# Kernel tuning notes

Hardware: AMD Instinct MI355X
Metric: run time of the kernel (lower is better)

Reference implementation:

```python
import jax, jax.numpy as jnp
import numpy as np

B, L, D = 2, 2048, 2048
NH, HD = 16, 128
SCALE = HD ** -0.5


def setup_inputs() -> dict:
    key = jax.random.key(0)
    ks = jax.random.split(key, 9)
    s = D ** -0.5  # roughly torch Linear init scale
    return {
        "hidden_states": jax.random.normal(ks[0], (B, L, D), dtype=jnp.float32),
        "Wq": jax.random.normal(ks[1], (NH * HD, D), dtype=jnp.float32) * s,
        "bq": jnp.zeros((NH * HD,), dtype=jnp.float32),
        "Wk": jax.random.normal(ks[2], (NH * HD, D), dtype=jnp.float32) * s,
        "bk": jnp.zeros((NH * HD,), dtype=jnp.float32),
        "Wv": jax.random.normal(ks[3], (NH * HD, D), dtype=jnp.float32) * s,
        "bv": jnp.zeros((NH * HD,), dtype=jnp.float32),
        "Wo": jax.random.normal(ks[4], (D, NH * HD), dtype=jnp.float32) * s,
        "bo": jnp.zeros((D,), dtype=jnp.float32),
    }


def reference(hidden_states, Wq, bq, Wk, bk, Wv, bv, Wo, bo):
    # projections (torch Linear: x @ W.T + b), split into heads: b s h d
    q = (hidden_states @ Wq.T + bq).reshape(B, L, NH, HD)
    k = (hidden_states @ Wk.T + bk).reshape(B, L, NH, HD)
    v = (hidden_states @ Wv.T + bv).reshape(B, L, NH, HD)
    # scores: [B, NH, L, L]
    scores = jnp.einsum("bqhd,bkhd->bhqk", q, k) * SCALE
    causal = jnp.tril(jnp.ones((L, L), dtype=bool))  # True = keep
    scores = jnp.where(causal, scores, jnp.float32(-jnp.inf))
    probs = jax.nn.softmax(scores, axis=-1)
    out = jnp.einsum("bhqk,bkhd->bqhd", probs, v).reshape(B, L, NH * HD)
    return out @ Wo.T + bo
```

## Files before the change

### kernel.cpp

```cpp
#include <hip/hip_runtime.h>

#define B_  2
#define L_  2048
#define D_  2048
#define NH_ 16
#define HD_ 128

typedef __bf16 bf16_t;
typedef __bf16 bf16x8 __attribute__((ext_vector_type(8)));
typedef __bf16 bf16x4 __attribute__((ext_vector_type(4)));
typedef float  f32x4  __attribute__((ext_vector_type(4)));

typedef const __attribute__((address_space(1))) void* gas_ptr;
typedef __attribute__((address_space(3))) void* las_ptr;

__device__ __forceinline__ void g2l16(const void* g, void* l) {
    __builtin_amdgcn_global_load_lds((gas_ptr)g, (las_ptr)l, 16, 0, 0);
}

__device__ __forceinline__ void raw_barrier() {
    asm volatile("s_barrier" ::: "memory");
}
__device__ __forceinline__ void wait_vm8() {
    asm volatile("s_waitcnt vmcnt(8)" ::: "memory");
}
__device__ __forceinline__ void wait_vm2() {
    asm volatile("s_waitcnt vmcnt(2)" ::: "memory");
}
__device__ __forceinline__ void wait_vm0() {
    asm volatile("s_waitcnt vmcnt(0)" ::: "memory");
}

__global__ __launch_bounds__(256) void cvt_all(const float* __restrict__ X,
                                               const float* __restrict__ Wq,
                                               const float* __restrict__ Wk,
                                               const float* __restrict__ Wv,
                                               const float* __restrict__ Wo,
                                               bf16_t* __restrict__ Xb,
                                               bf16_t* __restrict__ Wqkvb,
                                               bf16_t* __restrict__ Wob) {
    int i = blockIdx.x * 256 + threadIdx.x;
    const float* src;
    bf16_t* dst;
    int off;
    if (i < 2097152) { src = X; dst = Xb; off = i; }
    else {
        int j = i - 2097152;
        int w = j >> 20;
        off = j & 1048575;
        src = (w == 0) ? Wq : (w == 1) ? Wk : (w == 2) ? Wv : Wo;
        dst = (w == 3) ? Wob : Wqkvb + (size_t)w * 4194304;
    }
    float4 v = ((const float4*)src)[off];
    bf16x4 o;
    o[0] = (bf16_t)v.x; o[1] = (bf16_t)v.y; o[2] = (bf16_t)v.z; o[3] = (bf16_t)v.w;
    ((bf16x4*)dst)[off] = o;
}

__global__ __launch_bounds__(512, 2) void gemm_qk(const bf16_t* __restrict__ A,
                                                  const bf16_t* __restrict__ Bw,
                                                  const float* __restrict__ b0,
                                                  const float* __restrict__ b1,
                                                  bf16_t* __restrict__ QK) {
    constexpr int K  = D_;
    constexpr int BK = 64;
    constexpr int NT = K / BK;
    __shared__ __align__(16) bf16_t smem[65536];

    const int tid  = threadIdx.x;
    const int wave = tid >> 6, lane = tid & 63;
    const int quad = lane >> 4, l16 = lane & 15;
    const int tm = blockIdx.y * 256, tn = blockIdx.x * 256;
    const int seg = tn >> 11;

    const int srow = tid >> 3;
    const int sg   = (tid & 7) ^ (srow & 7);
    const bf16_t* Ag = A  + (size_t)(tm + srow) * K + sg * 8;
    const bf16_t* Bg = Bw + (size_t)(tn + srow) * K + sg * 8;
    const int ldsw = wave * 512;

    auto stageA = [&](int t, int h) {
        bf16_t* l = smem + (t & 1) * 32768 + h * 8192 + ldsw;
        const bf16_t* g = Ag + (size_t)h * 128 * K + t * BK;
        g2l16(g, l);
        g2l16(g + (size_t)64 * K, l + 4096);
    };
    auto stageB = [&](int t, int h) {
        bf16_t* l = smem + (t & 1) * 32768 + 16384 + h * 8192 + ldsw;
        const bf16_t* g = Bg + (size_t)h * 128 * K + t * BK;
        g2l16(g, l);
        g2l16(g + (size_t)64 * K, l + 4096);
    };

    f32x4 acc[8][4] = {};

    stageA(0, 0); stageA(0, 1); stageB(0, 0); stageB(0, 1);

    const int abase_w = (wave >> 2) * 8192;
    const int bbase_w = 16384 + ((wave >> 1) & 1) * 8192;
    const int brow0   = (wave & 1) * 64;

    for (int t = 0; t < NT; ++t) {
        const int p = t & 1;
        const bf16_t* Ah = smem + p * 32768 + abase_w;
        const bf16_t* Bh = smem + p * 32768 + bbase_w;
        bf16x8 af[4][2], bfr[2][2], bfr2[2][2];

        raw_barrier();
        if (t + 1 < NT) { stageA(t + 1, 0); wait_vm2(); }
        else wait_vm0();
        raw_barrier();

#pragma unroll
        for (int mb = 0; mb < 4; ++mb)
#pragma unroll
            for (int ks = 0; ks < 2; ++ks) {
                const int row = mb * 16 + l16;
                af[mb][ks] = *(const bf16x8*)(Ah + row * 64 + (((ks * 4 + quad) ^ (row & 7)) << 3));
            }
#pragma unroll
        for (int nb = 0; nb < 2; ++nb)
#pragma unroll
            for (int ks = 0; ks < 2; ++ks) {
                const int row = brow0 + nb * 16 + l16;
                bfr[nb][ks] = *(const bf16x8*)(Bh + row * 64 + (((ks * 4 + quad) ^ (row & 7)) << 3));
            }
        __builtin_amdgcn_s_setprio(1);
#pragma unroll
        for (int mb = 0; mb < 4; ++mb)
#pragma unroll
            for (int nb = 0; nb < 2; ++nb)
#pragma unroll
                for (int ks = 0; ks < 2; ++ks)
                    acc[mb][nb] = __builtin_amdgcn_mfma_f32_16x16x32_bf16(af[mb][ks], bfr[nb][ks], acc[mb][nb], 0, 0, 0);
        __builtin_amdgcn_s_setprio(0);

        if (t + 1 < NT) stageA(t + 1, 1);
#pragma unroll
        for (int nb = 0; nb < 2; ++nb)
#pragma unroll
            for (int ks = 0; ks < 2; ++ks) {
                const int row = brow0 + (nb + 2) * 16 + l16;
                bfr2[nb][ks] = *(const bf16x8*)(Bh + row * 64 + (((ks * 4 + quad) ^ (row & 7)) << 3));
            }
        raw_barrier();
        __builtin_amdgcn_s_setprio(1);
#pragma unroll
        for (int mb = 0; mb < 4; ++mb)
#pragma unroll
            for (int nb = 0; nb < 2; ++nb)
#pragma unroll
                for (int ks = 0; ks < 2; ++ks)
                    acc[mb][nb + 2] = __builtin_amdgcn_mfma_f32_16x16x32_bf16(af[mb][ks], bfr2[nb][ks], acc[mb][nb + 2], 0, 0, 0);
        __builtin_amdgcn_s_setprio(0);

        if (t + 1 < NT) stageB(t + 1, 0);
#pragma unroll
        for (int mb = 0; mb < 4; ++mb)
#pragma unroll
            for (int ks = 0; ks < 2; ++ks) {
                const int row = (mb + 4) * 16 + l16;
                af[mb][ks] = *(const bf16x8*)(Ah + row * 64 + (((ks * 4 + quad) ^ (row & 7)) << 3));
            }
        raw_barrier();
        __builtin_amdgcn_s_setprio(1);
#pragma unroll
        for (int mb = 0; mb < 4; ++mb)
#pragma unroll
            for (int nb = 0; nb < 2; ++nb)
#pragma unroll
                for (int ks = 0; ks < 2; ++ks)
                    acc[mb + 4][nb + 2] = __builtin_amdgcn_mfma_f32_16x16x32_bf16(af[mb][ks], bfr2[nb][ks], acc[mb + 4][nb + 2], 0, 0, 0);
        __builtin_amdgcn_s_setprio(0);

        if (t + 1 < NT) stageB(t + 1, 1);
#pragma unroll
        for (int nb = 0; nb < 2; ++nb)
#pragma unroll
            for (int ks = 0; ks < 2; ++ks) {
                const int row = brow0 + nb * 16 + l16;
                bfr[nb][ks] = *(const bf16x8*)(Bh + row * 64 + (((ks * 4 + quad) ^ (row & 7)) << 3));
            }
        raw_barrier();
        __builtin_amdgcn_s_setprio(1);
#pragma unroll
        for (int mb = 0; mb < 4; ++mb)
#pragma unroll
            for (int nb = 0; nb < 2; ++nb)
#pragma unroll
                for (int ks = 0; ks < 2; ++ks)
                    acc[mb + 4][nb] = __builtin_amdgcn_mfma_f32_16x16x32_bf16(af[mb][ks], bfr[nb][ks], acc[mb + 4][nb], 0, 0, 0);
        __builtin_amdgcn_s_setprio(0);
    }

    const int wm = (wave >> 2) * 128;
    const int wn = (wave & 3) * 64;
    const float* bias = (seg == 0) ? b0 : b1;
#pragma unroll
    for (int nb = 0; nb < 4; ++nb) {
        const int col = tn + wn + nb * 16 + l16;
        const float bv = bias[col & 2047];
#pragma unroll
        for (int mb = 0; mb < 8; ++mb) {
            const int row0 = tm + wm + mb * 16 + quad * 4;
#pragma unroll
            for (int r = 0; r < 4; ++r)
                QK[(size_t)(row0 + r) * 4096 + col] = (bf16_t)(acc[mb][nb][r] + bv);
        }
    }
}

__global__ __launch_bounds__(512, 2) void gemm_v(const bf16_t* __restrict__ A,
                                                 const bf16_t* __restrict__ Bv,
                                                 const float* __restrict__ b2,
                                                 bf16_t* __restrict__ Vt) {
    constexpr int K  = D_;
    constexpr int BK = 64;
    constexpr int NT = K / BK;
    __shared__ __align__(16) bf16_t smem[49152];

    const int tid  = threadIdx.x;
    const int wave = tid >> 6, lane = tid & 63;
    const int quad = lane >> 4, l16 = lane & 15;
    const int hx = blockIdx.x;
    const int tm = blockIdx.y * 256;
    const int wm = (wave >> 1) * 64;
    const int wn = (wave & 1) * 64;

    const int srow = tid >> 3;
    const int sg   = (tid & 7) ^ (srow & 7);
    const bf16_t* Ag = A  + (size_t)(tm + srow) * K + sg * 8;
    const bf16_t* Bg = Bv + (size_t)(hx * 128 + srow) * K + sg * 8;
    const int ldsw = wave * 512;

    auto stageVA = [&](int t, int q) {
        bf16_t* l = smem + (t & 1) * 24576 + q * 4096 + ldsw;
        g2l16(Ag + (size_t)q * 64 * K + t * BK, l);
    };
    auto stageVB = [&](int t, int q) {
        bf16_t* l = smem + (t & 1) * 24576 + 16384 + q * 4096 + ldsw;
        g2l16(Bg + (size_t)q * 64 * K + t * BK, l);
    };

    f32x4 acc[4][4] = {};

    stageVA(0, 0); stageVA(0, 1); stageVA(0, 2); stageVA(0, 3);
    stageVB(0, 0); stageVB(0, 1);

    for (int t = 0; t < NT; ++t) {
        const int p = t & 1;
        const bf16_t* Ah = smem + p * 24576;
        const bf16_t* Bl = smem + p * 24576 + 16384;
        bf16x8 af0[4], af1[4], bf0[2], bf1[2], bf2[2], bf3[2];

        raw_barrier();
        if (t + 1 < NT) { stageVA(t + 1, 0); stageVA(t + 1, 1); wait_vm2(); }
        else wait_vm0();
        raw_barrier();

#pragma unroll
        for (int mb = 0; mb < 4; ++mb) {
            const int row = wm + mb * 16 + l16;
            af0[mb] = *(const bf16x8*)(Ah + row * 64 + ((quad ^ (row & 7)) << 3));
        }
#pragma unroll
        for (int nb = 0; nb < 2; ++nb) {
            const int row = wn + nb * 16 + l16;
            bf0[nb] = *(const bf16x8*)(Bl + row * 64 + ((quad ^ (row & 7)) << 3));
        }
        __builtin_amdgcn_s_setprio(1);
#pragma unroll
        for (int mb = 0; mb < 4; ++mb)
#pragma unroll
            for (int nb = 0; nb < 2; ++nb)
                acc[mb][nb] = __builtin_amdgcn_mfma_f32_16x16x32_bf16(af0[mb], bf0[nb], acc[mb][nb], 0, 0, 0);
        __builtin_amdgcn_s_setprio(0);

        if (t + 1 < NT) { stageVA(t + 1, 2); stageVB(t + 1, 0); }
#pragma unroll
        for (int nb = 0; nb < 2; ++nb) {
            const int row = wn + (nb + 2) * 16 + l16;
            bf1[nb] = *(const bf16x8*)(Bl + row * 64 + ((quad ^ (row & 7)) << 3));
        }
        raw_barrier();
        __builtin_amdgcn_s_setprio(1);
#pragma unroll
        for (int mb = 0; mb < 4; ++mb)
#pragma unroll
            for (int nb = 0; nb < 2; ++nb)
                acc[mb][nb + 2] = __builtin_amdgcn_mfma_f32_16x16x32_bf16(af0[mb], bf1[nb], acc[mb][nb + 2], 0, 0, 0);
        __builtin_amdgcn_s_setprio(0);

        if (t + 1 < NT) { stageVA(t + 1, 3); stageVB(t + 1, 1); }
#pragma unroll
        for (int mb = 0; mb < 4; ++mb) {
            const int row = wm + mb * 16 + l16;
            af1[mb] = *(const bf16x8*)(Ah + row * 64 + (((4 + quad) ^ (row & 7)) << 3));
        }
#pragma unroll
        for (int nb = 0; nb < 2; ++nb) {
            const int row = wn + (nb + 2) * 16 + l16;
            bf2[nb] = *(const bf16x8*)(Bl + row * 64 + (((4 + quad) ^ (row & 7)) << 3));
        }
        raw_barrier();
        __builtin_amdgcn_s_setprio(1);
#pragma unroll
        for (int mb = 0; mb < 4; ++mb)
#pragma unroll
            for (int nb = 0; nb < 2; ++nb)
                acc[mb][nb + 2] = __builtin_amdgcn_mfma_f32_16x16x32_bf16(af1[mb], bf2[nb], acc[mb][nb + 2], 0, 0, 0);
        __builtin_amdgcn_s_setprio(0);

#pragma unroll
        for (int nb = 0; nb < 2; ++nb) {
            const int row = wn + nb * 16 + l16;
            bf3[nb] = *(const bf16x8*)(Bl + row * 64 + (((4 + quad) ^ (row & 7)) << 3));
        }
        raw_barrier();
        __builtin_amdgcn_s_setprio(1);
#pragma unroll
        for (int mb = 0; mb < 4; ++mb)
#pragma unroll
            for (int nb = 0; nb < 2; ++nb)
                acc[mb][nb] = __builtin_amdgcn_mfma_f32_16x16x32_bf16(af1[mb], bf3[nb], acc[mb][nb], 0, 0, 0);
        __builtin_amdgcn_s_setprio(0);
    }

    __syncthreads();
    bf16_t* Tw = smem + wave * 4096;
    const int b = tm >> 11;
    const int tokbase = tm & 2047;
#pragma unroll
    for (int nb = 0; nb < 4; ++nb) {
        const int dloc = nb * 16 + l16;
        const float bv = b2[hx * 128 + wn + dloc];
#pragma unroll
        for (int mb = 0; mb < 4; ++mb)
#pragma unroll
            for (int r = 0; r < 4; ++r) {
                const int tokl = mb * 16 + quad * 4 + r;
                Tw[dloc * 64 + ((((tokl >> 3) ^ (dloc & 7)) << 3) | (tokl & 7))] =
                    (bf16_t)(acc[mb][nb][r] + bv);
            }
    }
    const int dl = lane;
    bf16_t* gp = Vt + ((size_t)(b * NH_ + hx) * HD_ + wn + dl) * L_ + tokbase + wm;
#pragma unroll
    for (int c = 0; c < 8; ++c) {
        bf16x8 v = *(const bf16x8*)(Tw + dl * 64 + ((c ^ (dl & 7)) << 3));
        *(bf16x8*)(gp + c * 8) = v;
    }
}

__global__ __launch_bounds__(512, 2) void gemm_o(const bf16_t* __restrict__ A,
                                                 const bf16_t* __restrict__ Bw,
                                                 const float* __restrict__ bias,
                                                 float* __restrict__ C) {
    constexpr int K  = D_;
    constexpr int BK = 64;
    constexpr int NT = K / BK;
    __shared__ __align__(16) bf16_t smem[49152];

    const int tid  = threadIdx.x;
    const int wave = tid >> 6, lane = tid & 63;
    const int quad = lane >> 4, l16 = lane & 15;
    const int tn = blockIdx.x * 128;
    const int tm = blockIdx.y * 256;
    const int wm = (wave >> 1) * 64;
    const int wn = (wave & 1) * 64;

    const int srow = tid >> 3;
    const int sg   = (tid & 7) ^ (srow & 7);
    const bf16_t* Ag = A  + (size_t)(tm + srow) * K + sg * 8;
    const bf16_t* Bg = Bw + (size_t)(tn + srow) * K + sg * 8;
    const int ldsw = wave * 512;

    auto stageVA = [&](int t, int q) {
        bf16_t* l = smem + (t & 1) * 24576 + q * 4096 + ldsw;
        g2l16(Ag + (size_t)q * 64 * K + t * BK, l);
    };
    auto stageVB = [&](int t, int q) {
        bf16_t* l = smem + (t & 1) * 24576 + 16384 + q * 4096 + ldsw;
        g2l16(Bg + (size_t)q * 64 * K + t * BK, l);
    };

    f32x4 acc[4][4] = {};

    stageVA(0, 0); stageVA(0, 1); stageVA(0, 2); stageVA(0, 3);
    stageVB(0, 0); stageVB(0, 1);

    for (int t = 0; t < NT; ++t) {
        const int p = t & 1;
        const bf16_t* Ah = smem + p * 24576;
        const bf16_t* Bl = smem + p * 24576 + 16384;
        bf16x8 af0[4], af1[4], bf0[2], bf1[2], bf2[2], bf3[2];

        raw_barrier();
        if (t + 1 < NT) { stageVA(t + 1, 0); stageVA(t + 1, 1); wait_vm2(); }
        else wait_vm0();
        raw_barrier();

#pragma unroll
        for (int mb = 0; mb < 4; ++mb) {
            const int row = wm + mb * 16 + l16;
            af0[mb] = *(const bf16x8*)(Ah + row * 64 + ((quad ^ (row & 7)) << 3));
        }
#pragma unroll
        for (int nb = 0; nb < 2; ++nb) {
            const int row = wn + nb * 16 + l16;
            bf0[nb] = *(const bf16x8*)(Bl + row * 64 + ((quad ^ (row & 7)) << 3));
        }
        __builtin_amdgcn_s_setprio(1);
#pragma unroll
        for (int mb = 0; mb < 4; ++mb)
#pragma unroll
            for (int nb = 0; nb < 2; ++nb)
                acc[mb][nb] = __builtin_amdgcn_mfma_f32_16x16x32_bf16(af0[mb], bf0[nb], acc[mb][nb], 0, 0, 0);
        __builtin_amdgcn_s_setprio(0);

        if (t + 1 < NT) { stageVA(t + 1, 2); stageVB(t + 1, 0); }
#pragma unroll
        for (int nb = 0; nb < 2; ++nb) {
            const int row = wn + (nb + 2) * 16 + l16;
            bf1[nb] = *(const bf16x8*)(Bl + row * 64 + ((quad ^ (row & 7)) << 3));
        }
        raw_barrier();
        __builtin_amdgcn_s_setprio(1);
#pragma unroll
        for (int mb = 0; mb < 4; ++mb)
#pragma unroll
            for (int nb = 0; nb < 2; ++nb)
                acc[mb][nb + 2] = __builtin_amdgcn_mfma_f32_16x16x32_bf16(af0[mb], bf1[nb], acc[mb][nb + 2], 0, 0, 0);
        __builtin_amdgcn_s_setprio(0);

        if (t + 1 < NT) { stageVA(t + 1, 3); stageVB(t + 1, 1); }
#pragma unroll
        for (int mb = 0; mb < 4; ++mb) {
            const int row = wm + mb * 16 + l16;
            af1[mb] = *(const bf16x8*)(Ah + row * 64 + (((4 + quad) ^ (row & 7)) << 3));
        }
#pragma unroll
        for (int nb = 0; nb < 2; ++nb) {
            const int row = wn + (nb + 2) * 16 + l16;
            bf2[nb] = *(const bf16x8*)(Bl + row * 64 + (((4 + quad) ^ (row & 7)) << 3));
        }
        raw_barrier();
        __builtin_amdgcn_s_setprio(1);
#pragma unroll
        for (int mb = 0; mb < 4; ++mb)
#pragma unroll
            for (int nb = 0; nb < 2; ++nb)
                acc[mb][nb + 2] = __builtin_amdgcn_mfma_f32_16x16x32_bf16(af1[mb], bf2[nb], acc[mb][nb + 2], 0, 0, 0);
        __builtin_amdgcn_s_setprio(0);

#pragma unroll
        for (int nb = 0; nb < 2; ++nb) {
            const int row = wn + nb * 16 + l16;
            bf3[nb] = *(const bf16x8*)(Bl + row * 64 + (((4 + quad) ^ (row & 7)) << 3));
        }
        raw_barrier();
        __builtin_amdgcn_s_setprio(1);
#pragma unroll
        for (int mb = 0; mb < 4; ++mb)
#pragma unroll
            for (int nb = 0; nb < 2; ++nb)
                acc[mb][nb] = __builtin_amdgcn_mfma_f32_16x16x32_bf16(af1[mb], bf3[nb], acc[mb][nb], 0, 0, 0);
        __builtin_amdgcn_s_setprio(0);
    }

#pragma unroll
    for (int nb = 0; nb < 4; ++nb) {
        const int col = tn + wn + nb * 16 + l16;
        const float bv = bias[col];
#pragma unroll
        for (int mb = 0; mb < 4; ++mb) {
            const int row0 = tm + wm + mb * 16 + quad * 4;
#pragma unroll
            for (int r = 0; r < 4; ++r)
                C[(size_t)(row0 + r) * 2048 + col] = acc[mb][nb][r] + bv;
        }
    }
}

__global__ __launch_bounds__(256, 2) void attn_kernel(const bf16_t* __restrict__ QK,
                                                      const bf16_t* __restrict__ Vt,
                                                      bf16_t* __restrict__ Ctx) {
    constexpr float SCALE = 0.08838834764831845f;
    constexpr float MFIX  = 8.0f;
    const int bid = blockIdx.x;
    const int bh = bid & 31;
    const int qt = 15 - (bid >> 5);
    const int b = bh >> 4, h = bh & 15;
    const int tid = threadIdx.x, wave = tid >> 6, lane = tid & 63;
    const int quad = lane >> 4, l16 = lane & 15;
    const int q0 = qt * 128;

    __shared__ bf16_t Kl[2][64 * 128];
    __shared__ bf16_t Vl[2][128 * 64];
    __shared__ bf16_t Pl[4][16 * 72];

    bf16x8 qf[2][4];
#pragma unroll
    for (int s = 0; s < 2; ++s) {
        const bf16_t* qp = QK + (size_t)(b * L_ + q0 + wave * 32 + s * 16 + l16) * 4096 + h * HD_ + quad * 8;
#pragma unroll
        for (int ks = 0; ks < 4; ++ks) qf[s][ks] = *(const bf16x8*)(qp + ks * 32);
    }

    bf16x8 ones;
#pragma unroll
    for (int j = 0; j < 8; ++j) ones[j] = (bf16_t)1.0f;

    f32x4 oacc[2][8] = {};
    f32x4 lacc[2] = {};

    const bf16_t* Kg = QK + (size_t)(b * L_) * 4096 + 2048 + h * HD_;
    const bf16_t* Vg = Vt + (size_t)(bh * HD_) * L_;

    auto stage = [&](int tile, int p) {
        const bf16_t* kg = Kg + (size_t)tile * 64 * 4096;
        const bf16_t* vg = Vg + tile * 64;
#pragma unroll
        for (int c = 0; c < 4; ++c) {
            int row = c * 16 + wave * 4 + (lane >> 4);
            int gcol = ((lane & 15) ^ (row & 15)) * 8;
            g2l16(kg + (size_t)row * 4096 + gcol, &Kl[p][(c * 16 + wave * 4) * 128]);
        }
#pragma unroll
        for (int c = 0; c < 4; ++c) {
            int row = c * 32 + wave * 8 + (lane >> 3);
            int gcol = ((lane & 7) ^ (row & 7)) * 8;
            g2l16(vg + (size_t)row * L_ + gcol, &Vl[p][(c * 32 + wave * 8) * 64]);
        }
    };

    const int n = 2 * qt + 2;
    stage(0, 0);

    for (int it = 0; it < n; ++it) {
        const int p = it & 1;
        if (it + 1 < n) {
            stage(it + 1, p ^ 1);
            wait_vm8();
        } else {
            wait_vm0();
        }
        raw_barrier();

        const int kb = it * 64;
        const bool need_mask = (it >= n - 2);

        f32x4 sa[2][4] = {};
#pragma unroll
        for (int nt = 0; nt < 4; ++nt) {
            const int krow = nt * 16 + l16;
#pragma unroll
            for (int ks = 0; ks < 4; ++ks) {
                bf16x8 kf = *(const bf16x8*)(&Kl[p][krow * 128 + (((ks * 4 + quad) ^ l16) * 8)]);
                sa[0][nt] = __builtin_amdgcn_mfma_f32_16x16x32_bf16(qf[0][ks], kf, sa[0][nt], 0, 0, 0);
                sa[1][nt] = __builtin_amdgcn_mfma_f32_16x16x32_bf16(qf[1][ks], kf, sa[1][nt], 0, 0, 0);
            }
        }

        bf16x8 pf0[2], pf1[2];
#pragma unroll
        for (int nt = 0; nt < 4; ++nt)
#pragma unroll
            for (int r = 0; r < 4; ++r) {
                float sv = sa[0][nt][r] * SCALE - MFIX;
                if (need_mask) {
                    const int key = kb + nt * 16 + l16;
                    const int qq = q0 + wave * 32 + quad * 4 + r;
                    sv = (key <= qq) ? sv : -1e30f;
                }
                Pl[wave][(quad * 4 + r) * 72 + nt * 16 + l16] = (bf16_t)__expf(sv);
            }
        pf0[0] = *(const bf16x8*)(&Pl[wave][l16 * 72 + quad * 8]);
        pf0[1] = *(const bf16x8*)(&Pl[wave][l16 * 72 + 32 + quad * 8]);

#pragma unroll
        for (int nt = 0; nt < 4; ++nt)
#pragma unroll
            for (int r = 0; r < 4; ++r) {
                float sv = sa[1][nt][r] * SCALE - MFIX;
                if (need_mask) {
                    const int key = kb + nt * 16 + l16;
                    const int qq = q0 + wave * 32 + 16 + quad * 4 + r;
                    sv = (key <= qq) ? sv : -1e30f;
                }
                Pl[wave][(quad * 4 + r) * 72 + nt * 16 + l16] = (bf16_t)__expf(sv);
            }
        pf1[0] = *(const bf16x8*)(&Pl[wave][l16 * 72 + quad * 8]);
        pf1[1] = *(const bf16x8*)(&Pl[wave][l16 * 72 + 32 + quad * 8]);

        lacc[0] = __builtin_amdgcn_mfma_f32_16x16x32_bf16(pf0[0], ones, lacc[0], 0, 0, 0);
        lacc[0] = __builtin_amdgcn_mfma_f32_16x16x32_bf16(pf0[1], ones, lacc[0], 0, 0, 0);
        lacc[1] = __builtin_amdgcn_mfma_f32_16x16x32_bf16(pf1[0], ones, lacc[1], 0, 0, 0);
        lacc[1] = __builtin_amdgcn_mfma_f32_16x16x32_bf16(pf1[1], ones, lacc[1], 0, 0, 0);

#pragma unroll
        for (int dt = 0; dt < 8; ++dt) {
            const int drow = dt * 16 + l16;
#pragma unroll
            for (int ks = 0; ks < 2; ++ks) {
                bf16x8 vf = *(const bf16x8*)(&Vl[p][drow * 64 + (((ks * 4 + quad) ^ (drow & 7)) * 8)]);
                oacc[0][dt] = __builtin_amdgcn_mfma_f32_16x16x32_bf16(pf0[ks], vf, oacc[0][dt], 0, 0, 0);
                oacc[1][dt] = __builtin_amdgcn_mfma_f32_16x16x32_bf16(pf1[ks], vf, oacc[1][dt], 0, 0, 0);
            }
        }
        raw_barrier();
    }

#pragma unroll
    for (int s = 0; s < 2; ++s)
#pragma unroll
        for (int r = 0; r < 4; ++r) {
            const float inv = 1.0f / lacc[s][r];
            const int q = q0 + wave * 32 + s * 16 + quad * 4 + r;
            bf16_t* cp = Ctx + (size_t)(b * L_ + q) * 2048 + h * HD_;
#pragma unroll
            for (int dt = 0; dt < 8; ++dt)
                cp[dt * 16 + l16] = (bf16_t)(oacc[s][dt][r] * inv);
        }
}

extern "C" void kernel_launch(void* const* d_in, const int* in_sizes, int n_in,
                              void* d_out, int out_size, void* d_ws, size_t ws_size,
                              hipStream_t stream) {
    const float* X  = (const float*)d_in[0];
    const float* Wq = (const float*)d_in[1];
    const float* bq = (const float*)d_in[2];
    const float* Wk = (const float*)d_in[3];
    const float* bk = (const float*)d_in[4];
    const float* Wv = (const float*)d_in[5];
    const float* bv = (const float*)d_in[6];
    const float* Wo = (const float*)d_in[7];
    const float* bo = (const float*)d_in[8];
    float* out = (float*)d_out;

    char* ws = (char*)d_ws;
    bf16_t* Xb   = (bf16_t*)(ws);
    bf16_t* Ctx  = (bf16_t*)(ws);
    bf16_t* Wqkv = (bf16_t*)(ws + 16777216);
    bf16_t* Wob  = (bf16_t*)(ws + 41943040);
    bf16_t* QKb  = (bf16_t*)(ws + 50331648);
    bf16_t* Vtb  = (bf16_t*)(ws + 83886080);

    cvt_all<<<24576, 256, 0, stream>>>(X, Wq, Wk, Wv, Wo, Xb, Wqkv, Wob);

    gemm_qk<<<dim3(16, 16), 512, 0, stream>>>(Xb, Wqkv, bq, bk, QKb);

    gemm_v<<<dim3(16, 16), 512, 0, stream>>>(Xb, Wqkv + 8388608, bv, Vtb);

    attn_kernel<<<dim3(512), 256, 0, stream>>>(QKb, Vtb, Ctx);

    gemm_o<<<dim3(16, 16), 512, 0, stream>>>(Ctx, Wob, bo, out);
}
```

Baseline: 363.0 us.

## Merge QK and V projection GEMMs into one launch; reorder attention score MFMAs

The separate QK and V projection kernels become a single 512-block launch that branches on block index, so V-projection blocks can run alongside QK blocks and fill the tail of the first grid. The attention inner loop now keeps the K fragments in registers, finishes the first query sub-tile's scores, exp and row-sum before computing the second sub-tile's scores, and uses fmaf for the scale-and-shift. This aims to overlap the exp/LDS work with MFMA and cut one launch boundary, at the cost of more registers and a shared-memory footprint sized for the larger branch.

Result: faster. 351.1 us (-3.3%).

```diff
diff --git a/kernel.cpp b/kernel.cpp
--- a/kernel.cpp
+++ b/kernel.cpp
@@ -57,298 +57,286 @@
     ((bf16x4*)dst)[off] = o;
 }
 
-__global__ __launch_bounds__(512, 2) void gemm_qk(const bf16_t* __restrict__ A,
-                                                  const bf16_t* __restrict__ Bw,
-                                                  const float* __restrict__ b0,
-                                                  const float* __restrict__ b1,
-                                                  bf16_t* __restrict__ QK) {
+__global__ __launch_bounds__(512, 2) void gemm_qkv(const bf16_t* __restrict__ A,
+                                                   const bf16_t* __restrict__ Bw,
+                                                   const float* __restrict__ b0,
+                                                   const float* __restrict__ b1,
+                                                   const float* __restrict__ b2,
+                                                   bf16_t* __restrict__ QK,
+                                                   bf16_t* __restrict__ Vt) {
     constexpr int K  = D_;
     constexpr int BK = 64;
     constexpr int NT = K / BK;
     __shared__ __align__(16) bf16_t smem[65536];
 
+    const int bid = blockIdx.x;
     const int tid  = threadIdx.x;
     const int wave = tid >> 6, lane = tid & 63;
     const int quad = lane >> 4, l16 = lane & 15;
-    const int tm = blockIdx.y * 256, tn = blockIdx.x * 256;
-    const int seg = tn >> 11;
-
     const int srow = tid >> 3;
     const int sg   = (tid & 7) ^ (srow & 7);
-    const bf16_t* Ag = A  + (size_t)(tm + srow) * K + sg * 8;
-    const bf16_t* Bg = Bw + (size_t)(tn + srow) * K + sg * 8;
     const int ldsw = wave * 512;
 
-    auto stageA = [&](int t, int h) {
-        bf16_t* l = smem + (t & 1) * 32768 + h * 8192 + ldsw;
-        const bf16_t* g = Ag + (size_t)h * 128 * K + t * BK;
-        g2l16(g, l);
-        g2l16(g + (size_t)64 * K, l + 4096);
-    };
-    auto stageB = [&](int t, int h) {
-        bf16_t* l = smem + (t & 1) * 32768 + 16384 + h * 8192 + ldsw;
-        const bf16_t* g = Bg + (size_t)h * 128 * K + t * BK;
-        g2l16(g, l);
-        g2l16(g + (size_t)64 * K, l + 4096);
-    };
-
-    f32x4 acc[8][4] = {};
-
-    stageA(0, 0); stageA(0, 1); stageB(0, 0); stageB(0, 1);
-
-    const int abase_w = (wave >> 2) * 8192;
-    const int bbase_w = 16384 + ((wave >> 1) & 1) * 8192;
-    const int brow0   = (wave & 1) * 64;
-
-    for (int t = 0; t < NT; ++t) {
-        const int p = t & 1;
-        const bf16_t* Ah = smem + p * 32768 + abase_w;
-        const bf16_t* Bh = smem + p * 32768 + bbase_w;
-        bf16x8 af[4][2], bfr[2][2], bfr2[2][2];
-
-        raw_barrier();
-        if (t + 1 < NT) { stageA(t + 1, 0); wait_vm2(); }
-        else wait_vm0();
-        raw_barrier();
-
-#pragma unroll
-        for (int mb = 0; mb < 4; ++mb)
-#pragma unroll
-            for (int ks = 0; ks < 2; ++ks) {
-                const int row = mb * 16 + l16;
-                af[mb][ks] = *(const bf16x8*)(Ah + row * 64 + (((ks * 4 + quad) ^ (row & 7)) << 3));
-            }
-#pragma unroll
-        for (int nb = 0; nb < 2; ++nb)
-#pragma unroll
-            for (int ks = 0; ks < 2; ++ks) {
-                const int row = brow0 + nb * 16 + l16;
-                bfr[nb][ks] = *(const bf16x8*)(Bh + row * 64 + (((ks * 4 + quad) ^ (row & 7)) << 3));
-            }
-        __builtin_amdgcn_s_setprio(1);
-#pragma unroll
-        for (int mb = 0; mb < 4; ++mb)
+    if (bid < 256) {
+        const int tm = (bid >> 4) * 256, tn = (bid & 15) * 256;
+        const int seg = tn >> 11;
+        const bf16_t* Ag = A  + (size_t)(tm + srow) * K + sg * 8;
+        const bf16_t* Bg = Bw + (size_t)(tn + srow) * K + sg * 8;
+
+        auto stageA = [&](int t, int h) {
+            bf16_t* l = smem + (t & 1) * 32768 + h * 8192 + ldsw;
+            const bf16_t* g = Ag + (size_t)h * 128 * K + t * BK;
+            g2l16(g, l);
+            g2l16(g + (size_t)64 * K, l + 4096);
+        };
+        auto stageB = [&](int t, int h) {
+            bf16_t* l = smem + (t & 1) * 32768 + 16384 + h * 8192 + ldsw;
+            const bf16_t* g = Bg + (size_t)h * 128 * K + t * BK;
+            g2l16(g, l);
+            g2l16(g + (size_t)64 * K, l + 4096);
+        };
+
+        f32x4 acc[8][4] = {};
+        stageA(0, 0); stageA(0, 1); stageB(0, 0); stageB(0, 1);
+
+        const int abase_w = (wave >> 2) * 8192;
+        const int bbase_w = 16384 + ((wave >> 1) & 1) * 8192;
+        const int brow0   = (wave & 1) * 64;
+
+        for (int t = 0; t < NT; ++t) {
+            const int p = t & 1;
+            const bf16_t* Ah = smem + p * 32768 + abase_w;
+            const bf16_t* Bh = smem + p * 32768 + bbase_w;
+            bf16x8 af[4][2], bfr[2][2], bfr2[2][2];
+
+            raw_barrier();
+            if (t + 1 < NT) { stageA(t + 1, 0); wait_vm2(); }
+            else wait_vm0();
+            raw_barrier();
+
+#pragma unroll
+            for (int mb = 0; mb < 4; ++mb)
+#pragma unroll
+                for (int ks = 0; ks < 2; ++ks) {
+                    const int row = mb * 16 + l16;
+                    af[mb][ks] = *(const bf16x8*)(Ah + row * 64 + (((ks * 4 + quad) ^ (row & 7)) << 3));
+                }
 #pragma unroll
             for (int nb = 0; nb < 2; ++nb)
 #pragma unroll
-                for (int ks = 0; ks < 2; ++ks)
-                    acc[mb][nb] = __builtin_amdgcn_mfma_f32_16x16x32_bf16(af[mb][ks], bfr[nb][ks], acc[mb][nb], 0, 0, 0);
-        __builtin_amdgcn_s_setprio(0);
-
-        if (t + 1 < NT) stageA(t + 1, 1);
-#pragma unroll
-        for (int nb = 0; nb < 2; ++nb)
-#pragma unroll
-            for (int ks = 0; ks < 2; ++ks) {
-                const int row = brow0 + (nb + 2) * 16 + l16;
-                bfr2[nb][ks] = *(const bf16x8*)(Bh + row * 64 + (((ks * 4 + quad) ^ (row & 7)) << 3));
-            }
-        raw_barrier();
-        __builtin_amdgcn_s_setprio(1);
-#pragma unroll
-        for (int mb = 0; mb < 4; ++mb)
+                for (int ks = 0; ks < 2; ++ks) {
+                    const int row = brow0 + nb * 16 + l16;
+                    bfr[nb][ks] = *(const bf16x8*)(Bh + row * 64 + (((ks * 4 + quad) ^ (row & 7)) << 3));
+                }
+            __builtin_amdgcn_s_setprio(1);
+#pragma unroll
+            for (int mb = 0; mb < 4; ++mb)
+#pragma unroll
+                for (int nb = 0; nb < 2; ++nb)
+#pragma unroll
+                    for (int ks = 0; ks < 2; ++ks)
+                        acc[mb][nb] = __builtin_amdgcn_mfma_f32_16x16x32_bf16(af[mb][ks], bfr[nb][ks], acc[mb][nb], 0, 0, 0);
+            __builtin_amdgcn_s_setprio(0);
+
+            if (t + 1 < NT) stageA(t + 1, 1);
 #pragma unroll
             for (int nb = 0; nb < 2; ++nb)
 #pragma unroll
-                for (int ks = 0; ks < 2; ++ks)
-                    acc[mb][nb + 2] = __builtin_amdgcn_mfma_f32_16x16x32_bf16(af[mb][ks], bfr2[nb][ks], acc[mb][nb + 2], 0, 0, 0);
-        __builtin_amdgcn_s_setprio(0);
-
-        if (t + 1 < NT) stageB(t + 1, 0);
-#pragma unroll
-        for (int mb = 0; mb < 4; ++mb)
-#pragma unroll
-            for (int ks = 0; ks < 2; ++ks) {
-                const int row = (mb + 4) * 16 + l16;
-                af[mb][ks] = *(const bf16x8*)(Ah + row * 64 + (((ks * 4 + quad) ^ (row & 7)) << 3));
-            }
-        raw_barrier();
-        __builtin_amdgcn_s_setprio(1);
-#pragma unroll
-        for (int mb = 0; mb < 4; ++mb)
+                for (int ks = 0; ks < 2; ++ks) {
+                    const int row = brow0 + (nb + 2) * 16 + l16;
+                    bfr2[nb][ks] = *(const bf16x8*)(Bh + row * 64 + (((ks * 4 + quad) ^ (row & 7)) << 3));
+                }
+            raw_barrier();
+            __builtin_amdgcn_s_setprio(1);
+#pragma unroll
+            for (int mb = 0; mb < 4; ++mb)
+#pragma unroll
+                for (int nb = 0; nb < 2; ++nb)
+#pragma unroll
+                    for (int ks = 0; ks < 2; ++ks)
+                        acc[mb][nb + 2] = __builtin_amdgcn_mfma_f32_16x16x32_bf16(af[mb][ks], bfr2[nb][ks], acc[mb][nb + 2], 0, 0, 0);
+            __builtin_amdgcn_s_setprio(0);
+
+            if (t + 1 < NT) stageB(t + 1, 0);
+#pragma unroll
+            for (int mb = 0; mb < 4; ++mb)
+#pragma unroll
+                for (int ks = 0; ks < 2; ++ks) {
+                    const int row = (mb + 4) * 16 + l16;
+                    af[mb][ks] = *(const bf16x8*)(Ah + row * 64 + (((ks * 4 + quad) ^ (row & 7)) << 3));
+                }
+            raw_barrier();
+            __builtin_amdgcn_s_setprio(1);
+#pragma unroll
+            for (int mb = 0; mb < 4; ++mb)
+#pragma unroll
+                for (int nb = 0; nb < 2; ++nb)
+#pragma unroll
+                    for (int ks = 0; ks < 2; ++ks)
+                        acc[mb + 4][nb + 2] = __builtin_amdgcn_mfma_f32_16x16x32_bf16(af[mb][ks], bfr2[nb][ks], acc[mb + 4][nb + 2], 0, 0, 0);
+            __builtin_amdgcn_s_setprio(0);
+
+            if (t + 1 < NT) stageB(t + 1, 1);
 #pragma unroll
             for (int nb = 0; nb < 2; ++nb)
 #pragma unroll
-                for (int ks = 0; ks < 2; ++ks)
-                    acc[mb + 4][nb + 2] = __builtin_amdgcn_mfma_f32_16x16x32_bf16(af[mb][ks], bfr2[nb][ks], acc[mb + 4][nb + 2], 0, 0, 0);
-        __builtin_amdgcn_s_setprio(0);
-
-        if (t + 1 < NT) stageB(t + 1, 1);
-#pragma unroll
-        for (int nb = 0; nb < 2; ++nb)
-#pragma unroll
-            for (int ks = 0; ks < 2; ++ks) {
-                const int row = brow0 + nb * 16 + l16;
-                bfr[nb][ks] = *(const bf16x8*)(Bh + row * 64 + (((ks * 4 + quad) ^ (row & 7)) << 3));
-            }
-        raw_barrier();
-        __builtin_amdgcn_s_setprio(1);
-#pragma unroll
-        for (int mb = 0; mb < 4; ++mb)
-#pragma unroll
-            for (int nb = 0; nb < 2; ++nb)
-#pragma unroll
-                for (int ks = 0; ks < 2; ++ks)
-                    acc[mb + 4][nb] = __builtin_amdgcn_mfma_f32_16x16x32_bf16(af[mb][ks], bfr[nb][ks], acc[mb + 4][nb], 0, 0, 0);
-        __builtin_amdgcn_s_setprio(0);
-    }
-
-    const int wm = (wave >> 2) * 128;
-    const int wn = (wave & 3) * 64;
-    const float* bias = (seg == 0) ? b0 : b1;
-#pragma unroll
-    for (int nb = 0; nb < 4; ++nb) {
-        const int col = tn + wn + nb * 16 + l16;
-        const float bv = bias[col & 2047];
-#pragma unroll
-        for (int mb = 0; mb < 8; ++mb) {
-            const int row0 = tm + wm + mb * 16 + quad * 4;
-#pragma unroll
-            for (int r = 0; r < 4; ++r)
-                QK[(size_t)(row0 + r) * 4096 + col] = (bf16_t)(acc[mb][nb][r] + bv);
-        }
-    }
-}
-
-__global__ __launch_bounds__(512, 2) void gemm_v(const bf16_t* __restrict__ A,
-                                                 const bf16_t* __restrict__ Bv,
-                                                 const float* __restrict__ b2,
-                                                 bf16_t* __restrict__ Vt) {
-    constexpr int K  = D_;
-    constexpr int BK = 64;
-    constexpr int NT = K / BK;
-    __shared__ __align__(16) bf16_t smem[49152];
-
-    const int tid  = threadIdx.x;
-    const int wave = tid >> 6, lane = tid & 63;
-    const int quad = lane >> 4, l16 = lane & 15;
-    const int hx = blockIdx.x;
-    const int tm = blockIdx.y * 256;
-    const int wm = (wave >> 1) * 64;
-    const int wn = (wave & 1) * 64;
-
-    const int srow = tid >> 3;
-    const int sg   = (tid & 7) ^ (srow & 7);
-    const bf16_t* Ag = A  + (size_t)(tm + srow) * K + sg * 8;
-    const bf16_t* Bg = Bv + (size_t)(hx * 128 + srow) * K + sg * 8;
-    const int ldsw = wave * 512;
-
-    auto stageVA = [&](int t, int q) {
-        bf16_t* l = smem + (t & 1) * 24576 + q * 4096 + ldsw;
-        g2l16(Ag + (size_t)q * 64 * K + t * BK, l);
-    };
-    auto stageVB = [&](int t, int q) {
-        bf16_t* l = smem + (t & 1) * 24576 + 16384 + q * 4096 + ldsw;
-        g2l16(Bg + (size_t)q * 64 * K + t * BK, l);
-    };
-
-    f32x4 acc[4][4] = {};
-
-    stageVA(0, 0); stageVA(0, 1); stageVA(0, 2); stageVA(0, 3);
-    stageVB(0, 0); stageVB(0, 1);
-
-    for (int t = 0; t < NT; ++t) {
-        const int p = t & 1;
-        const bf16_t* Ah = smem + p * 24576;
-        const bf16_t* Bl = smem + p * 24576 + 16384;
-        bf16x8 af0[4], af1[4], bf0[2], bf1[2], bf2[2], bf3[2];
-
-        raw_barrier();
-        if (t + 1 < NT) { stageVA(t + 1, 0); stageVA(t + 1, 1); wait_vm2(); }
-        else wait_vm0();
-        raw_barrier();
-
-#pragma unroll
-        for (int mb = 0; mb < 4; ++mb) {
-            const int row = wm + mb * 16 + l16;
-            af0[mb] = *(const bf16x8*)(Ah + row * 64 + ((quad ^ (row & 7)) << 3));
-        }
-#pragma unroll
-        for (int nb = 0; nb < 2; ++nb) {
-            const int row = wn + nb * 16 + l16;
-            bf0[nb] = *(const bf16x8*)(Bl + row * 64 + ((quad ^ (row & 7)) << 3));
-        }
-        __builtin_amdgcn_s_setprio(1);
-#pragma unroll
-        for (int mb = 0; mb < 4; ++mb)
-#pragma unroll
-            for (int nb = 0; nb < 2; ++nb)
-                acc[mb][nb] = __builtin_amdgcn_mfma_f32_16x16x32_bf16(af0[mb], bf0[nb], acc[mb][nb], 0, 0, 0);
-        __builtin_amdgcn_s_setprio(0);
-
-        if (t + 1 < NT) { stageVA(t + 1, 2); stageVB(t + 1, 0); }
-#pragma unroll
-        for (int nb = 0; nb < 2; ++nb) {
-            const int row = wn + (nb + 2) * 16 + l16;
-            bf1[nb] = *(const bf16x8*)(Bl + row * 64 + ((quad ^ (row & 7)) << 3));
-        }
-        raw_barrier();
-        __builtin_amdgcn_s_setprio(1);
-#pragma unroll
-        for (int mb = 0; mb < 4; ++mb)
-#pragma unroll
-            for (int nb = 0; nb < 2; ++nb)
-                acc[mb][nb + 2] = __builtin_amdgcn_mfma_f32_16x16x32_bf16(af0[mb], bf1[nb], acc[mb][nb + 2], 0, 0, 0);
-        __builtin_amdgcn_s_setprio(0);
-
-        if (t + 1 < NT) { stageVA(t + 1, 3); stageVB(t + 1, 1); }
-#pragma unroll
-        for (int mb = 0; mb < 4; ++mb) {
-            const int row = wm + mb * 16 + l16;
-            af1[mb] = *(const bf16x8*)(Ah + row * 64 + (((4 + quad) ^ (row & 7)) << 3));
-        }
-#pragma unroll
-        for (int nb = 0; nb < 2; ++nb) {
-            const int row = wn + (nb + 2) * 16 + l16;
-            bf2[nb] = *(const bf16x8*)(Bl + row * 64 + (((4 + quad) ^ (row & 7)) << 3));
-        }
-        raw_barrier();
-        __builtin_amdgcn_s_setprio(1);
-#pragma unroll
-        for (int mb = 0; mb < 4; ++mb)
-#pragma unroll
-            for (int nb = 0; nb < 2; ++nb)
-                acc[mb][nb + 2] = __builtin_amdgcn_mfma_f32_16x16x32_bf16(af1[mb], bf2[nb], acc[mb][nb + 2], 0, 0, 0);
-        __builtin_amdgcn_s_setprio(0);
-
-#pragma unroll
-        for (int nb = 0; nb < 2; ++nb) {
-            const int row = wn + nb * 16 + l16;
-            bf3[nb] = *(const bf16x8*)(Bl + row * 64 + (((4 + quad) ^ (row & 7)) << 3));
-        }
-        raw_barrier();
-        __builtin_amdgcn_s_setprio(1);
-#pragma unroll
-        for (int mb = 0; mb < 4; ++mb)
-#pragma unroll
-            for (int nb = 0; nb < 2; ++nb)
-                acc[mb][nb] = __builtin_amdgcn_mfma_f32_16x16x32_bf16(af1[mb], bf3[nb], acc[mb][nb], 0, 0, 0);
-        __builtin_amdgcn_s_setprio(0);
-    }
-
-    __syncthreads();
-    bf16_t* Tw = smem + wave * 4096;
-    const int b = tm >> 11;
-    const int tokbase = tm & 2047;
-#pragma unroll
-    for (int nb = 0; nb < 4; ++nb) {
-        const int dloc = nb * 16 + l16;
-        const float bv = b2[hx * 128 + wn + dloc];
-#pragma unroll
-        for (int mb = 0; mb < 4; ++mb)
-#pragma unroll
-            for (int r = 0; r < 4; ++r) {
-                const int tokl = mb * 16 + quad * 4 + r;
-                Tw[dloc * 64 + ((((tokl >> 3) ^ (dloc & 7)) << 3) | (tokl & 7))] =
-                    (bf16_t)(acc[mb][nb][r] + bv);
-            }
-    }
-    const int dl = lane;
-    bf16_t* gp = Vt + ((size_t)(b * NH_ + hx) * HD_ + wn + dl) * L_ + tokbase + wm;
-#pragma unroll
-    for (int c = 0; c < 8; ++c) {
-        bf16x8 v = *(const bf16x8*)(Tw + dl * 64 + ((c ^ (dl & 7)) << 3));
-        *(bf16x8*)(gp + c * 8) = v;
+                for (int ks = 0; ks < 2; ++ks) {
+                    const int row = brow0 + nb * 16 + l16;
+                    bfr[nb][ks] = *(const bf16x8*)(Bh + row * 64 + (((ks * 4 + quad) ^ (row & 7)) << 3));
+                }
+            raw_barrier();
+            __builtin_amdgcn_s_setprio(1);
+#pragma unroll
+            for (int mb = 0; mb < 4; ++mb)
+#pragma unroll
+                for (int nb = 0; nb < 2; ++nb)
+#pragma unroll
+                    for (int ks = 0; ks < 2; ++ks)
+                        acc[mb + 4][nb] = __builtin_amdgcn_mfma_f32_16x16x32_bf16(af[mb][ks], bfr[nb][ks], acc[mb + 4][nb], 0, 0, 0);
+            __builtin_amdgcn_s_setprio(0);
+        }
+
+        const int wm = (wave >> 2) * 128;
+        const int wn = (wave & 3) * 64;
+        const float* bias = (seg == 0) ? b0 : b1;
+#pragma unroll
+        for (int nb = 0; nb < 4; ++nb) {
+            const int col = tn + wn + nb * 16 + l16;
+            const float bv = bias[col & 2047];
+#pragma unroll
+            for (int mb = 0; mb < 8; ++mb) {
+                const int row0 = tm + wm + mb * 16 + quad * 4;
+#pragma unroll
+                for (int r = 0; r < 4; ++r)
+                    QK[(size_t)(row0 + r) * 4096 + col] = (bf16_t)(acc[mb][nb][r] + bv);
+            }
+        }
+    } else {
+        const int vb = bid - 256;
+        const int hx = vb & 15;
+        const int tm = (vb >> 4) * 256;
+        const int wm = (wave >> 1) * 64;
+        const int wn = (wave & 1) * 64;
+
+        const bf16_t* Ag = A + (size_t)(tm + srow) * K + sg * 8;
+        const bf16_t* Bg = Bw + 8388608 + (size_t)(hx * 128 + srow) * K + sg * 8;
+
+        auto stageVA = [&](int t, int q) {
+            bf16_t* l = smem + (t & 1) * 24576 + q * 4096 + ldsw;
+            g2l16(Ag + (size_t)q * 64 * K + t * BK, l);
+        };
+        auto stageVB = [&](int t, int q) {
+            bf16_t* l = smem + (t & 1) * 24576 + 16384 + q * 4096 + ldsw;
+            g2l16(Bg + (size_t)q * 64 * K + t * BK, l);
+        };
+
+        f32x4 acc[4][4] = {};
+        stageVA(0, 0); stageVA(0, 1); stageVA(0, 2); stageVA(0, 3);
+        stageVB(0, 0); stageVB(0, 1);
+
+        for (int t = 0; t < NT; ++t) {
+            const int p = t & 1;
+            const bf16_t* Ah = smem + p * 24576;
+            const bf16_t* Bl = smem + p * 24576 + 16384;
+            bf16x8 af0[4], af1[4], bf0[2], bf1[2], bf2[2], bf3[2];
+
+            raw_barrier();
+            if (t + 1 < NT) { stageVA(t + 1, 0); stageVA(t + 1, 1); wait_vm2(); }
+            else wait_vm0();
+            raw_barrier();
+
+#pragma unroll
+            for (int mb = 0; mb < 4; ++mb) {
+                const int row = wm + mb * 16 + l16;
+                af0[mb] = *(const bf16x8*)(Ah + row * 64 + ((quad ^ (row & 7)) << 3));
+            }
+#pragma unroll
+            for (int nb = 0; nb < 2; ++nb) {
+                const int row = wn + nb * 16 + l16;
+                bf0[nb] = *(const bf16x8*)(Bl + row * 64 + ((quad ^ (row & 7)) << 3));
+            }
+            __builtin_amdgcn_s_setprio(1);
+#pragma unroll
+            for (int mb = 0; mb < 4; ++mb)
+#pragma unroll
+                for (int nb = 0; nb < 2; ++nb)
+                    acc[mb][nb] = __builtin_amdgcn_mfma_f32_16x16x32_bf16(af0[mb], bf0[nb], acc[mb][nb], 0, 0, 0);
+            __builtin_amdgcn_s_setprio(0);
+
+            if (t + 1 < NT) { stageVA(t + 1, 2); stageVB(t + 1, 0); }
+#pragma unroll
+            for (int nb = 0; nb < 2; ++nb) {
+                const int row = wn + (nb + 2) * 16 + l16;
+                bf1[nb] = *(const bf16x8*)(Bl + row * 64 + ((quad ^ (row & 7)) << 3));
+            }
+            raw_barrier();
+            __builtin_amdgcn_s_setprio(1);
+#pragma unroll
+            for (int mb = 0; mb < 4; ++mb)
+#pragma unroll
+                for (int nb = 0; nb < 2; ++nb)
+                    acc[mb][nb + 2] = __builtin_amdgcn_mfma_f32_16x16x32_bf16(af0[mb], bf1[nb], acc[mb][nb + 2], 0, 0, 0);
+            __builtin_amdgcn_s_setprio(0);
+
+            if (t + 1 < NT) { stageVA(t + 1, 3); stageVB(t + 1, 1); }
+#pragma unroll
+            for (int mb = 0; mb < 4; ++mb) {
+                const int row = wm + mb * 16 + l16;
+                af1[mb] = *(const bf16x8*)(Ah + row * 64 + (((4 + quad) ^ (row & 7)) << 3));
+            }
+#pragma unroll
+            for (int nb = 0; nb < 2; ++nb) {
+                const int row = wn + (nb + 2) * 16 + l16;
+                bf2[nb] = *(const bf16x8*)(Bl + row * 64 + (((4 + quad) ^ (row & 7)) << 3));
+            }
+            raw_barrier();
+            __builtin_amdgcn_s_setprio(1);
+#pragma unroll
+            for (int mb = 0; mb < 4; ++mb)
+#pragma unroll
+                for (int nb = 0; nb < 2; ++nb)
+                    acc[mb][nb + 2] = __builtin_amdgcn_mfma_f32_16x16x32_bf16(af1[mb], bf2[nb], acc[mb][nb + 2], 0, 0, 0);
+            __builtin_amdgcn_s_setprio(0);
+
+#pragma unroll
+            for (int nb = 0; nb < 2; ++nb) {
+                const int row = wn + nb * 16 + l16;
+                bf3[nb] = *(const bf16x8*)(Bl + row * 64 + (((4 + quad) ^ (row & 7)) << 3));
+            }
+            raw_barrier();
+            __builtin_amdgcn_s_setprio(1);
+#pragma unroll
+            for (int mb = 0; mb < 4; ++mb)
+#pragma unroll
+                for (int nb = 0; nb < 2; ++nb)
+                    acc[mb][nb] = __builtin_amdgcn_mfma_f32_16x16x32_bf16(af1[mb], bf3[nb], acc[mb][nb], 0, 0, 0);
+            __builtin_amdgcn_s_setprio(0);
+        }
+
+        __syncthreads();
+        bf16_t* Tw = smem + wave * 4096;
+        const int b = tm >> 11;
+        const int tokbase = tm & 2047;
+#pragma unroll
+        for (int nb = 0; nb < 4; ++nb) {
+            const int dloc = nb * 16 + l16;
+            const float bv = b2[hx * 128 + wn + dloc];
+#pragma unroll
+            for (int mb = 0; mb < 4; ++mb)
+#pragma unroll
+                for (int r = 0; r < 4; ++r) {
+                    const int tokl = mb * 16 + quad * 4 + r;
+                    Tw[dloc * 64 + ((((tokl >> 3) ^ (dloc & 7)) << 3) | (tokl & 7))] =
+                        (bf16_t)(acc[mb][nb][r] + bv);
+                }
+        }
+        const int dl = lane;
+        bf16_t* gp = Vt + ((size_t)(b * NH_ + hx) * HD_ + wn + dl) * L_ + tokbase + wm;
+#pragma unroll
+        for (int c = 0; c < 8; ++c) {
+            bf16x8 v = *(const bf16x8*)(Tw + dl * 64 + ((c ^ (dl & 7)) << 3));
+            *(bf16x8*)(gp + c * 8) = v;
+        }
     }
 }
 
@@ -550,15 +538,15 @@
         const int kb = it * 64;
         const bool need_mask = (it >= n - 2);
 
-        f32x4 sa[2][4] = {};
+        bf16x8 kfr[4][4];
+        f32x4 sa0[4] = {}, sa1[4] = {};
 #pragma unroll
         for (int nt = 0; nt < 4; ++nt) {
             const int krow = nt * 16 + l16;
 #pragma unroll
             for (int ks = 0; ks < 4; ++ks) {
-                bf16x8 kf = *(const bf16x8*)(&Kl[p][krow * 128 + (((ks * 4 + quad) ^ l16) * 8)]);
-                sa[0][nt] = __builtin_amdgcn_mfma_f32_16x16x32_bf16(qf[0][ks], kf, sa[0][nt], 0, 0, 0);
-                sa[1][nt] = __builtin_amdgcn_mfma_f32_16x16x32_bf16(qf[1][ks], kf, sa[1][nt], 0, 0, 0);
+                kfr[nt][ks] = *(const bf16x8*)(&Kl[p][krow * 128 + (((ks * 4 + quad) ^ l16) * 8)]);
+                sa0[nt] = __builtin_amdgcn_mfma_f32_16x16x32_bf16(qf[0][ks], kfr[nt][ks], sa0[nt], 0, 0, 0);
             }
         }
 
@@ -567,7 +555,7 @@
         for (int nt = 0; nt < 4; ++nt)
 #pragma unroll
             for (int r = 0; r < 4; ++r) {
-                float sv = sa[0][nt][r] * SCALE - MFIX;
+                float sv = fmaf(sa0[nt][r], SCALE, -MFIX);
                 if (need_mask) {
                     const int key = kb + nt * 16 + l16;
                     const int qq = q0 + wave * 32 + quad * 4 + r;
@@ -577,12 +565,20 @@
             }
         pf0[0] = *(const bf16x8*)(&Pl[wave][l16 * 72 + quad * 8]);
         pf0[1] = *(const bf16x8*)(&Pl[wave][l16 * 72 + 32 + quad * 8]);
+        lacc[0] = __builtin_amdgcn_mfma_f32_16x16x32_bf16(pf0[0], ones, lacc[0], 0, 0, 0);
+        lacc[0] = __builtin_amdgcn_mfma_f32_16x16x32_bf16(pf0[1], ones, lacc[0], 0, 0, 0);
 
 #pragma unroll
         for (int nt = 0; nt < 4; ++nt)
 #pragma unroll
+            for (int ks = 0; ks < 4; ++ks)
+                sa1[nt] = __builtin_amdgcn_mfma_f32_16x16x32_bf16(qf[1][ks], kfr[nt][ks], sa1[nt], 0, 0, 0);
+
+#pragma unroll
+        for (int nt = 0; nt < 4; ++nt)
+#pragma unroll
             for (int r = 0; r < 4; ++r) {
-                float sv = sa[1][nt][r] * SCALE - MFIX;
+                float sv = fmaf(sa1[nt][r], SCALE, -MFIX);
                 if (need_mask) {
                     const int key = kb + nt * 16 + l16;
                     const int qq = q0 + wave * 32 + 16 + quad * 4 + r;
@@ -592,9 +588,6 @@
             }
         pf1[0] = *(const bf16x8*)(&Pl[wave][l16 * 72 + quad * 8]);
         pf1[1] = *(const bf16x8*)(&Pl[wave][l16 * 72 + 32 + quad * 8]);
-
-        lacc[0] = __builtin_amdgcn_mfma_f32_16x16x32_bf16(pf0[0], ones, lacc[0], 0, 0, 0);
-        lacc[0] = __builtin_amdgcn_mfma_f32_16x16x32_bf16(pf0[1], ones, lacc[0], 0, 0, 0);
         lacc[1] = __builtin_amdgcn_mfma_f32_16x16x32_bf16(pf1[0], ones, lacc[1], 0, 0, 0);
         lacc[1] = __builtin_amdgcn_mfma_f32_16x16x32_bf16(pf1[1], ones, lacc[1], 0, 0, 0);
 
@@ -648,9 +641,7 @@
 
     cvt_all<<<24576, 256, 0, stream>>>(X, Wq, Wk, Wv, Wo, Xb, Wqkv, Wob);
 
-    gemm_qk<<<dim3(16, 16), 512, 0, stream>>>(Xb, Wqkv, bq, bk, QKb);
-
-    gemm_v<<<dim3(16, 16), 512, 0, stream>>>(Xb, Wqkv + 8388608, bv, Vtb);
+    gemm_qkv<<<dim3(512), 512, 0, stream>>>(Xb, Wqkv, bq, bk, bv, QKb, Vtb);
 
     attn_kernel<<<dim3(512), 256, 0, stream>>>(QKb, Vtb, Ctx);
 
```
